# Performance work log

Measured on AMD Instinct MI355X. Metric: run time of the kernel, lower is better.

The kernel has to match this reference:

```python
import jax, jax.numpy as jnp
import numpy as np

HIDDEN = 1024
NUM_HEADS = 16
HEAD = HIDDEN // NUM_HEADS
B, S = 2, 2048


def setup_inputs() -> dict:
    key = jax.random.key(0)
    ks = jax.random.split(key, 7)
    scale = 1.0 / np.sqrt(HIDDEN)
    return {
        "hidden_states": jax.random.normal(ks[0], (B, S, HIDDEN), dtype=jnp.float32),
        "Wq": jax.random.normal(ks[1], (HIDDEN, HIDDEN), dtype=jnp.float32) * scale,
        "bq": jax.random.normal(ks[2], (HIDDEN,), dtype=jnp.float32) * 0.01,
        "Wk": jax.random.normal(ks[3], (HIDDEN, HIDDEN), dtype=jnp.float32) * scale,
        "bk": jax.random.normal(ks[4], (HIDDEN,), dtype=jnp.float32) * 0.01,
        "Wv": jax.random.normal(ks[5], (HIDDEN, HIDDEN), dtype=jnp.float32) * scale,
        "bv": jax.random.normal(ks[6], (HIDDEN,), dtype=jnp.float32) * 0.01,
    }


def _split_heads(x):
    b, s, _ = x.shape
    return x.reshape(b, s, NUM_HEADS, HEAD).transpose(0, 2, 1, 3)  # [B,H,S,D]


def reference(hidden_states, Wq, bq, Wk, bk, Wv, bv):
    # Linear projections (dropout is inference no-op)
    Q = _split_heads(hidden_states @ Wq + bq)
    K = _split_heads(hidden_states @ Wk + bk)
    V = _split_heads(hidden_states @ Wv + bv)
    scores = jnp.einsum("bhqd,bhkd->bhqk", Q, K) / np.sqrt(HEAD).astype(np.float32)
    probs = jax.nn.softmax(scores, axis=-1)
    context = jnp.einsum("bhqk,bhkd->bhqd", probs, V)  # [B,H,S,D]
    return context.transpose(0, 2, 1, 3).reshape(B, S, HIDDEN)
```

## Files before the change

kernel.cpp:

```cpp
#include <hip/hip_runtime.h>
#include <hip/hip_bf16.h>

typedef __bf16 bf16_t;
typedef __bf16 bf16x4v __attribute__((ext_vector_type(4)));
typedef __bf16 bf16x8 __attribute__((ext_vector_type(8)));
typedef float f32x4 __attribute__((ext_vector_type(4)));
typedef float f32x16 __attribute__((ext_vector_type(16)));
typedef unsigned short u16;
typedef unsigned int u32;
typedef u16 u16x8 __attribute__((ext_vector_type(8)));

#define HIDDEN 1024
#define NHEAD 16
#define HEADD 64
#define BATCH 2
#define SEQ 2048
#define TOKENS (BATCH*SEQ)

#define M12F -12.0f
#define M16 {M12F,M12F,M12F,M12F,M12F,M12F,M12F,M12F,M12F,M12F,M12F,M12F,M12F,M12F,M12F,M12F}

__global__ __launch_bounds__(256) void k_transpose_w(const float* __restrict__ Wq,
                                                     const float* __restrict__ Wk,
                                                     const float* __restrict__ Wv,
                                                     bf16_t* __restrict__ wt) {
  int mat = blockIdx.z;
  const float* W = (mat == 0) ? Wq : (mat == 1 ? Wk : Wv);
  bf16_t* dst = wt + (size_t)mat * HIDDEN * HIDDEN;
  __shared__ float tile[32][33];
  int k0 = blockIdx.x * 32, n0 = blockIdx.y * 32;
  int tc = threadIdx.x & 31, tr = threadIdx.x >> 5;
#pragma unroll
  for (int r = 0; r < 32; r += 8)
    tile[tr + r][tc] = W[(size_t)(k0 + tr + r) * HIDDEN + n0 + tc];
  __syncthreads();
#pragma unroll
  for (int r = 0; r < 32; r += 8)
    dst[(size_t)(n0 + tr + r) * HIDDEN + k0 + tc] = (bf16_t)tile[tc][tr + r];
}

__global__ __launch_bounds__(512, 3) void k_gemm_qkv(
    const float* __restrict__ hs, const bf16_t* __restrict__ wt,
    const float* __restrict__ bq, const float* __restrict__ bk,
    const float* __restrict__ bv, bf16_t* __restrict__ Qo,
    bf16_t* __restrict__ Ko, bf16_t* __restrict__ Vo) {
  __shared__ bf16x8 As[2][4 * 128];
  __shared__ bf16x8 Bs[2][4 * 256];
  int t = threadIdx.x;
  int wave = t >> 6, lane = t & 63;
  int m0 = blockIdx.x * 128;
  int nb = blockIdx.y;
  int mat = nb >> 2;
  int n0 = (nb & 3) * 256;
  const bf16_t* Wmat = wt + (size_t)mat * HIDDEN * HIDDEN;
  const float* bias = (mat == 0) ? bq : (mat == 1 ? bk : bv);
  bf16_t* dst = (mat == 0) ? Qo : (mat == 1 ? Ko : Vo);

  int wm = wave >> 2, wn = wave & 3;
  int lrow = lane & 15;
  int lc = lane >> 4;

  f32x4 acc[4][4];
#pragma unroll
  for (int a = 0; a < 4; ++a)
#pragma unroll
    for (int b = 0; b < 4; ++b) acc[a][b] = (f32x4){0.f, 0.f, 0.f, 0.f};

  bf16x8 ra, rb[2];
  auto load_tiles = [&](int kt) {
    int k0 = kt * 32;
    {
      int row = t >> 2, c = t & 3;
      const float* ap = hs + (size_t)(m0 + row) * HIDDEN + k0 + c * 8;
      float4 f0 = *(const float4*)(ap);
      float4 f1 = *(const float4*)(ap + 4);
      bf16x8 v;
      v[0] = (bf16_t)f0.x; v[1] = (bf16_t)f0.y; v[2] = (bf16_t)f0.z; v[3] = (bf16_t)f0.w;
      v[4] = (bf16_t)f1.x; v[5] = (bf16_t)f1.y; v[6] = (bf16_t)f1.z; v[7] = (bf16_t)f1.w;
      ra = v;
    }
#pragma unroll
    for (int u = 0; u < 2; ++u) {
      int id = t + u * 512;
      int row = id >> 2, c = id & 3;
      rb[u] = *(const bf16x8*)(Wmat + (size_t)(n0 + row) * HIDDEN + k0 + c * 8);
    }
  };
  auto store_tiles = [&](int buf) {
    {
      int row = t >> 2, c = t & 3;
      As[buf][c * 128 + (row ^ c)] = ra;
    }
#pragma unroll
    for (int u = 0; u < 2; ++u) {
      int id = t + u * 512;
      int row = id >> 2, c = id & 3;
      Bs[buf][c * 256 + (row ^ c)] = rb[u];
    }
  };

  load_tiles(0);
  store_tiles(0);
  __syncthreads();
  const int NT = HIDDEN / 32;
  int cur = 0;
  for (int kt = 0; kt < NT; ++kt) {
    if (kt + 1 < NT) load_tiles(kt + 1);
    bf16x8 af[4], bfr[4];
#pragma unroll
    for (int fm = 0; fm < 4; ++fm)
      af[fm] = As[cur][lc * 128 + ((wm * 64 + fm * 16 + lrow) ^ lc)];
#pragma unroll
    for (int fn = 0; fn < 4; ++fn)
      bfr[fn] = Bs[cur][lc * 256 + ((wn * 64 + fn * 16 + lrow) ^ lc)];
#pragma unroll
    for (int fm = 0; fm < 4; ++fm)
#pragma unroll
      for (int fn = 0; fn < 4; ++fn)
        acc[fm][fn] = __builtin_amdgcn_mfma_f32_16x16x32_bf16(
            af[fm], bfr[fn], acc[fm][fn], 0, 0, 0);
    if (kt + 1 < NT) store_tiles(cur ^ 1);
    __syncthreads();
    cur ^= 1;
  }

  float scale = (mat == 0) ? 0.18033688011112042f : 1.0f;
#pragma unroll
  for (int fm = 0; fm < 4; ++fm) {
#pragma unroll
    for (int fn = 0; fn < 4; ++fn) {
      int n = n0 + wn * 64 + fn * 16 + (lane & 15);
      float bval = bias[n];
      int h = n >> 6, d = n & 63;
      int mbase = m0 + wm * 64 + fm * 16 + (lane >> 4) * 4;
      int b = mbase >> 11, s = mbase & 2047;
      if (mat == 2) {
        bf16x4v pk;
#pragma unroll
        for (int j = 0; j < 4; ++j) pk[j] = (bf16_t)(acc[fm][fn][j] + bval);
        *(bf16x4v*)(dst + ((size_t)(b * NHEAD + h) * HEADD + d) * SEQ + s) = pk;
      } else {
#pragma unroll
        for (int j = 0; j < 4; ++j) {
          float v = (acc[fm][fn][j] + bval) * scale;
          dst[((size_t)(b * NHEAD + h) * SEQ + (s + j)) * HEADD + d] = (bf16_t)v;
        }
      }
    }
  }
}

__device__ __forceinline__ void gload16(const void* g, void* l) {
  __builtin_amdgcn_global_load_lds((const __attribute__((address_space(1))) u32*)g,
                                   (__attribute__((address_space(3))) u32*)l, 16, 0, 0);
}

#define PACKSUM(sA, sB, PF, L)                                               \
  do {                                                                       \
    u32 u[16];                                                               \
    _Pragma("unroll")                                                        \
    for (int i = 0; i < 8; ++i) {                                            \
      union { bf16_t hh[2]; u32 ww; } c0, c1;                                \
      c0.hh[0] = (bf16_t)sA[2 * i]; c0.hh[1] = (bf16_t)sA[2 * i + 1];        \
      c1.hh[0] = (bf16_t)sB[2 * i]; c1.hh[1] = (bf16_t)sB[2 * i + 1];        \
      u[i] = c0.ww; u[8 + i] = c1.ww;                                        \
    }                                                                        \
    _Pragma("unroll")                                                        \
    for (int i = 0; i < 16; ++i)                                             \
      asm("v_dot2_f32_bf16 %0, %1, %2, %0"                                   \
          : "+v"(L) : "v"(u[i]), "v"(ones_));                                \
    _Pragma("unroll")                                                        \
    for (int gg = 0; gg < 4; ++gg) {                                         \
      u32 a0 = u[4 * gg + 0], b0 = u[4 * gg + 2];                            \
      u32 a1 = u[4 * gg + 1], b1 = u[4 * gg + 3];                            \
      asm("v_permlane32_swap_b32 %0, %1" : "+v"(a0), "+v"(b0));              \
      asm("v_permlane32_swap_b32 %0, %1" : "+v"(a1), "+v"(b1));              \
      union { u32 wv[4]; bf16x8 v; } fu;                                     \
      fu.wv[0] = a0; fu.wv[1] = a1; fu.wv[2] = b0; fu.wv[3] = b1;            \
      PF[gg] = fu.v;                                                         \
    }                                                                        \
  } while (0)

__global__ __launch_bounds__(256, 2) void k_attn(const bf16_t* __restrict__ Q,
                                                 const bf16_t* __restrict__ K,
                                                 const bf16_t* __restrict__ Vt,
                                                 float* __restrict__ out) {
  __shared__ __align__(16) char smem[66560];
  const int t = threadIdx.x;
  const int w = t >> 6, l = t & 63;
  const int g = w >> 1, qh = w & 1;
  const int hi = l >> 5;
  const int l31 = l & 31;
  const int lx = l & 7;

  const int n_hw = blockIdx.x + 16 * blockIdx.y;
  const int work = (n_hw & 7) * 64 + (n_hw >> 3);
  const int qt = work & 15;
  const int bh = work >> 4;
  const int b = bh >> 4, h = bh & 15;
  const char* Kp = (const char*)(K + (size_t)bh * SEQ * HEADD) + (size_t)g * 1024 * 128;
  const char* Vp = (const char*)(Vt + (size_t)bh * HEADD * SEQ) + (size_t)g * 1024 * 2;
  const bf16_t* Qp = Q + (size_t)bh * SEQ * HEADD;

  const int q0w = qt * 128 + qh * 64;

  bf16x8 qa0[4], qa1[4];
#pragma unroll
  for (int ds = 0; ds < 4; ++ds) {
    qa0[ds] = *(const bf16x8*)(Qp + (size_t)(q0w + l31) * HEADD + ds * 16 + hi * 8);
    qa1[ds] = *(const bf16x8*)(Qp + (size_t)(q0w + 32 + l31) * HEADD + ds * 16 + hi * 8);
  }

  f32x16 o00 = (f32x16)(0.f), o01 = (f32x16)(0.f);
  f32x16 o10 = (f32x16)(0.f), o11 = (f32x16)(0.f);
  float l_run0 = 0.f, l_run1 = 0.f;
  const u32 ones_ = 0x3F803F80u;

  char* gK = smem + g * 32768;
  char* gV = gK + 16384;
  const int srow = qh * 32 + (l >> 3);
  const int sg = lx ^ (l >> 3);

  auto stage = [&](int tile, int buf) {
#pragma unroll
    for (int s = 0; s < 4; ++s) {
      int row = srow + 8 * s;
      gload16(Kp + (size_t)(tile * 64 + row) * 128 + sg * 16,
              gK + buf * 8192 + qh * 4096 + s * 1024);
      gload16(Vp + (size_t)row * (SEQ * 2) + tile * 128 + sg * 16,
              gV + buf * 8192 + qh * 4096 + s * 1024);
    }
  };

  stage(0, 0);
  __syncthreads();

  int roff0[4], roff1[4];
#pragma unroll
  for (int ds = 0; ds < 4; ++ds) {
    roff0[ds] = l31 * 128 + ((2 * ds + hi) ^ lx) * 16;
    roff1[ds] = (32 + l31) * 128 + ((2 * ds + hi) ^ lx) * 16;
  }

  const f32x16 minit = M16;
  int cur = 0;
  for (int r = 0; r < 16; ++r) {
    if (r < 15) stage(r + 1, cur ^ 1);
    const char* Kc = gK + cur * 8192;
    const char* Vc = gV + cur * 8192;

    f32x16 s0 = minit, s1 = minit, s2 = minit, s3 = minit;
    __builtin_amdgcn_s_setprio(1);
#pragma unroll
    for (int ds = 0; ds < 4; ++ds) {
      bf16x8 kf0 = *(const bf16x8*)(Kc + roff0[ds]);
      bf16x8 kf1 = *(const bf16x8*)(Kc + roff1[ds]);
      s0 = __builtin_amdgcn_mfma_f32_32x32x16_bf16(kf0, qa0[ds], s0, 0, 0, 0);
      s1 = __builtin_amdgcn_mfma_f32_32x32x16_bf16(kf1, qa0[ds], s1, 0, 0, 0);
      s2 = __builtin_amdgcn_mfma_f32_32x32x16_bf16(kf0, qa1[ds], s2, 0, 0, 0);
      s3 = __builtin_amdgcn_mfma_f32_32x32x16_bf16(kf1, qa1[ds], s3, 0, 0, 0);
    }
    __builtin_amdgcn_s_setprio(0);

#pragma unroll
    for (int i = 0; i < 16; ++i) {
      s0[i] = __builtin_amdgcn_exp2f(s0[i]);
      s1[i] = __builtin_amdgcn_exp2f(s1[i]);
      s2[i] = __builtin_amdgcn_exp2f(s2[i]);
      s3[i] = __builtin_amdgcn_exp2f(s3[i]);
    }

    bf16x8 pf0[4], pf1[4];
    PACKSUM(s0, s1, pf0, l_run0);
    PACKSUM(s2, s3, pf1, l_run1);

    __builtin_amdgcn_s_setprio(1);
#pragma unroll
    for (int kblk = 0; kblk < 4; ++kblk) {
      bf16x8 vf0 = *(const bf16x8*)(Vc + roff0[kblk]);
      bf16x8 vf1 = *(const bf16x8*)(Vc + roff1[kblk]);
      o00 = __builtin_amdgcn_mfma_f32_32x32x16_bf16(vf0, pf0[kblk], o00, 0, 0, 0);
      o01 = __builtin_amdgcn_mfma_f32_32x32x16_bf16(vf1, pf0[kblk], o01, 0, 0, 0);
      o10 = __builtin_amdgcn_mfma_f32_32x32x16_bf16(vf0, pf1[kblk], o10, 0, 0, 0);
      o11 = __builtin_amdgcn_mfma_f32_32x32x16_bf16(vf1, pf1[kblk], o11, 0, 0, 0);
    }
    __builtin_amdgcn_s_setprio(0);
    __syncthreads();
    cur ^= 1;
  }

  float l_h0 = l_run0 + __shfl_xor(l_run0, 32);
  float l_h1 = l_run1 + __shfl_xor(l_run1, 32);
  float* OL = (float*)(smem + g * 32768);
  const int orow0 = qh * 64 + l31;
  const int orow1 = qh * 64 + 32 + l31;
#pragma unroll
  for (int j = 0; j < 16; ++j) {
    int dv0 = (j & 3) + 8 * (j >> 2) + 4 * hi;
    OL[orow0 * 64 + ((dv0 + orow0) & 63)] = o00[j];
    OL[orow0 * 64 + ((dv0 + 32 + orow0) & 63)] = o01[j];
    OL[orow1 * 64 + ((dv0 + orow1) & 63)] = o10[j];
    OL[orow1 * 64 + ((dv0 + 32 + orow1) & 63)] = o11[j];
  }
  float* LL = (float*)(smem + 65536);
  if (hi == 0) {
    LL[g * 128 + orow0] = l_h0;
    LL[g * 128 + orow1] = l_h1;
  }
  __syncthreads();
  {
    int ql = t >> 1;
    int dvb = (t & 1) * 32;
    float inv = 1.0f / (LL[ql] + LL[128 + ql]);
    const float* A = (const float*)smem;
    const float* B = (const float*)(smem + 32768);
    float* op = out + ((size_t)b * SEQ + qt * 128 + ql) * HIDDEN + h * HEADD + dvb;
#pragma unroll
    for (int g4 = 0; g4 < 8; ++g4) {
      f32x4 v4;
#pragma unroll
      for (int e = 0; e < 4; ++e) {
        int dv = dvb + g4 * 4 + e;
        int idx = ql * 64 + ((dv + ql) & 63);
        v4[e] = (A[idx] + B[idx]) * inv;
      }
      *(f32x4*)(op + g4 * 4) = v4;
    }
  }
}

extern "C" void kernel_launch(void* const* d_in, const int* in_sizes, int n_in,
                              void* d_out, int out_size, void* d_ws, size_t ws_size,
                              hipStream_t stream) {
  const float* hs = (const float*)d_in[0];
  const float* Wq = (const float*)d_in[1];
  const float* bq = (const float*)d_in[2];
  const float* Wk = (const float*)d_in[3];
  const float* bk = (const float*)d_in[4];
  const float* Wv = (const float*)d_in[5];
  const float* bv = (const float*)d_in[6];
  float* out = (float*)d_out;
  char* ws = (char*)d_ws;

  const size_t SZ_X = (size_t)TOKENS * HIDDEN * 2;
  const size_t SZ_W = (size_t)3 * HIDDEN * HIDDEN * 2;
  const size_t SZ_P = (size_t)TOKENS * HIDDEN * 2;
  bf16_t* Wt = (bf16_t*)(ws + SZ_X);
  bf16_t* Qb = (bf16_t*)(ws + SZ_X + SZ_W);
  bf16_t* Kb = (bf16_t*)(ws + SZ_X + SZ_W + SZ_P);
  bf16_t* Vb = (bf16_t*)(ws + SZ_X + SZ_W + 2 * SZ_P);

  k_transpose_w<<<dim3(32, 32, 3), 256, 0, stream>>>(Wq, Wk, Wv, Wt);
  k_gemm_qkv<<<dim3(32, 12), 512, 0, stream>>>(hs, Wt, bq, bk, bv, Qb, Kb, Vb);
  k_attn<<<dim3(16, 32), 256, 0, stream>>>(Qb, Kb, Vb, out);
}
```

Before: 97.46 us.

## Halve attention KV tile to 32 keys to fit four blocks per CU

Cuts the per-iteration key tile from 64 to 32 keys, which halves the LDS staging buffers and score registers and lets the launch bound request four blocks per CU instead of two. The V staging layout and swizzle are rewritten for the narrower tile. The final cross-group reduction now runs in two phases through a single LDS buffer, so LDS use fits in about 33KB. In exchange there are twice as many loop iterations and barriers, each with less MFMA work to hide load latency behind.

```diff
diff --git a/kernel.cpp b/kernel.cpp
--- a/kernel.cpp
+++ b/kernel.cpp
@@ -155,22 +155,21 @@
                                    (__attribute__((address_space(3))) u32*)l, 16, 0, 0);
 }
 
-#define PACKSUM(sA, sB, PF, L)                                               \
+#define PACKSUM32(sA, PF, L)                                                 \
   do {                                                                       \
-    u32 u[16];                                                               \
+    u32 u[8];                                                                \
     _Pragma("unroll")                                                        \
     for (int i = 0; i < 8; ++i) {                                            \
-      union { bf16_t hh[2]; u32 ww; } c0, c1;                                \
+      union { bf16_t hh[2]; u32 ww; } c0;                                    \
       c0.hh[0] = (bf16_t)sA[2 * i]; c0.hh[1] = (bf16_t)sA[2 * i + 1];        \
-      c1.hh[0] = (bf16_t)sB[2 * i]; c1.hh[1] = (bf16_t)sB[2 * i + 1];        \
-      u[i] = c0.ww; u[8 + i] = c1.ww;                                        \
+      u[i] = c0.ww;                                                          \
     }                                                                        \
     _Pragma("unroll")                                                        \
-    for (int i = 0; i < 16; ++i)                                             \
+    for (int i = 0; i < 8; ++i)                                              \
       asm("v_dot2_f32_bf16 %0, %1, %2, %0"                                   \
           : "+v"(L) : "v"(u[i]), "v"(ones_));                                \
     _Pragma("unroll")                                                        \
-    for (int gg = 0; gg < 4; ++gg) {                                         \
+    for (int gg = 0; gg < 2; ++gg) {                                         \
       u32 a0 = u[4 * gg + 0], b0 = u[4 * gg + 2];                            \
       u32 a1 = u[4 * gg + 1], b1 = u[4 * gg + 3];                            \
       asm("v_permlane32_swap_b32 %0, %1" : "+v"(a0), "+v"(b0));              \
@@ -181,11 +180,11 @@
     }                                                                        \
   } while (0)
 
-__global__ __launch_bounds__(256, 2) void k_attn(const bf16_t* __restrict__ Q,
+__global__ __launch_bounds__(256, 4) void k_attn(const bf16_t* __restrict__ Q,
                                                  const bf16_t* __restrict__ K,
                                                  const bf16_t* __restrict__ Vt,
                                                  float* __restrict__ out) {
-  __shared__ __align__(16) char smem[66560];
+  __shared__ __align__(16) char smem[33792];
   const int t = threadIdx.x;
   const int w = t >> 6, l = t & 63;
   const int g = w >> 1, qh = w & 1;
@@ -216,69 +215,67 @@
   float l_run0 = 0.f, l_run1 = 0.f;
   const u32 ones_ = 0x3F803F80u;
 
-  char* gK = smem + g * 32768;
-  char* gV = gK + 16384;
-  const int srow = qh * 32 + (l >> 3);
-  const int sg = lx ^ (l >> 3);
+  char* gK = smem + g * 16384;
+  char* gV = gK + 8192;
 
   auto stage = [&](int tile, int buf) {
 #pragma unroll
-    for (int s = 0; s < 4; ++s) {
-      int row = srow + 8 * s;
-      gload16(Kp + (size_t)(tile * 64 + row) * 128 + sg * 16,
-              gK + buf * 8192 + qh * 4096 + s * 1024);
-      gload16(Vp + (size_t)row * (SEQ * 2) + tile * 128 + sg * 16,
-              gV + buf * 8192 + qh * 4096 + s * 1024);
+    for (int s = 0; s < 2; ++s) {
+      int krow = qh * 16 + s * 8 + (l >> 3);
+      gload16(Kp + (size_t)(tile * 32 + krow) * 128 + (lx ^ (krow & 7)) * 16,
+              gK + buf * 4096 + qh * 2048 + s * 1024);
+      int vrow = qh * 32 + s * 16 + (l >> 2);
+      int vg = (l & 3) ^ (vrow & 3);
+      gload16(Vp + (size_t)vrow * (SEQ * 2) + tile * 64 + vg * 16,
+              gV + buf * 4096 + qh * 2048 + s * 1024);
     }
   };
 
   stage(0, 0);
   __syncthreads();
 
-  int roff0[4], roff1[4];
-#pragma unroll
-  for (int ds = 0; ds < 4; ++ds) {
-    roff0[ds] = l31 * 128 + ((2 * ds + hi) ^ lx) * 16;
-    roff1[ds] = (32 + l31) * 128 + ((2 * ds + hi) ^ lx) * 16;
+  int kroff[4], vroff0[2], vroff1[2];
+#pragma unroll
+  for (int ds = 0; ds < 4; ++ds)
+    kroff[ds] = l31 * 128 + ((2 * ds + hi) ^ lx) * 16;
+#pragma unroll
+  for (int kb = 0; kb < 2; ++kb) {
+    vroff0[kb] = l31 * 64 + ((2 * kb + hi) ^ (l31 & 3)) * 16;
+    vroff1[kb] = (32 + l31) * 64 + ((2 * kb + hi) ^ (l31 & 3)) * 16;
   }
 
   const f32x16 minit = M16;
   int cur = 0;
-  for (int r = 0; r < 16; ++r) {
-    if (r < 15) stage(r + 1, cur ^ 1);
-    const char* Kc = gK + cur * 8192;
-    const char* Vc = gV + cur * 8192;
-
-    f32x16 s0 = minit, s1 = minit, s2 = minit, s3 = minit;
+  for (int r = 0; r < 32; ++r) {
+    if (r < 31) stage(r + 1, cur ^ 1);
+    const char* Kc = gK + cur * 4096;
+    const char* Vc = gV + cur * 4096;
+
+    f32x16 s0 = minit, s2 = minit;
     __builtin_amdgcn_s_setprio(1);
 #pragma unroll
     for (int ds = 0; ds < 4; ++ds) {
-      bf16x8 kf0 = *(const bf16x8*)(Kc + roff0[ds]);
-      bf16x8 kf1 = *(const bf16x8*)(Kc + roff1[ds]);
-      s0 = __builtin_amdgcn_mfma_f32_32x32x16_bf16(kf0, qa0[ds], s0, 0, 0, 0);
-      s1 = __builtin_amdgcn_mfma_f32_32x32x16_bf16(kf1, qa0[ds], s1, 0, 0, 0);
-      s2 = __builtin_amdgcn_mfma_f32_32x32x16_bf16(kf0, qa1[ds], s2, 0, 0, 0);
-      s3 = __builtin_amdgcn_mfma_f32_32x32x16_bf16(kf1, qa1[ds], s3, 0, 0, 0);
+      bf16x8 kf = *(const bf16x8*)(Kc + kroff[ds]);
+      s0 = __builtin_amdgcn_mfma_f32_32x32x16_bf16(kf, qa0[ds], s0, 0, 0, 0);
+      s2 = __builtin_amdgcn_mfma_f32_32x32x16_bf16(kf, qa1[ds], s2, 0, 0, 0);
     }
     __builtin_amdgcn_s_setprio(0);
 
 #pragma unroll
     for (int i = 0; i < 16; ++i) {
       s0[i] = __builtin_amdgcn_exp2f(s0[i]);
-      s1[i] = __builtin_amdgcn_exp2f(s1[i]);
       s2[i] = __builtin_amdgcn_exp2f(s2[i]);
-      s3[i] = __builtin_amdgcn_exp2f(s3[i]);
-    }
-
-    bf16x8 pf0[4], pf1[4];
-    PACKSUM(s0, s1, pf0, l_run0);
-    PACKSUM(s2, s3, pf1, l_run1);
+    }
+
+    bf16x8 pf0[2], pf1[2];
+    PACKSUM32(s0, pf0, l_run0);
+    PACKSUM32(s2, pf1, l_run1);
 
     __builtin_amdgcn_s_setprio(1);
 #pragma unroll
-    for (int kblk = 0; kblk < 4; ++kblk) {
-      bf16x8 vf0 = *(const bf16x8*)(Vc + roff0[kblk]);
-      bf16x8 vf1 = *(const bf16x8*)(Vc + roff1[kblk]);
+    for (int kblk = 0; kblk < 2; ++kblk) {
+      bf16x8 vf0 = *(const bf16x8*)(Vc + vroff0[kblk]);
+      bf16x8 vf1 = *(const bf16x8*)(Vc + vroff1[kblk]);
       o00 = __builtin_amdgcn_mfma_f32_32x32x16_bf16(vf0, pf0[kblk], o00, 0, 0, 0);
       o01 = __builtin_amdgcn_mfma_f32_32x32x16_bf16(vf1, pf0[kblk], o01, 0, 0, 0);
       o10 = __builtin_amdgcn_mfma_f32_32x32x16_bf16(vf0, pf1[kblk], o10, 0, 0, 0);
@@ -291,29 +288,38 @@
 
   float l_h0 = l_run0 + __shfl_xor(l_run0, 32);
   float l_h1 = l_run1 + __shfl_xor(l_run1, 32);
-  float* OL = (float*)(smem + g * 32768);
+  float* OL = (float*)smem;
+  float* LL = (float*)(smem + 32768);
   const int orow0 = qh * 64 + l31;
   const int orow1 = qh * 64 + 32 + l31;
-#pragma unroll
-  for (int j = 0; j < 16; ++j) {
-    int dv0 = (j & 3) + 8 * (j >> 2) + 4 * hi;
-    OL[orow0 * 64 + ((dv0 + orow0) & 63)] = o00[j];
-    OL[orow0 * 64 + ((dv0 + 32 + orow0) & 63)] = o01[j];
-    OL[orow1 * 64 + ((dv0 + orow1) & 63)] = o10[j];
-    OL[orow1 * 64 + ((dv0 + 32 + orow1) & 63)] = o11[j];
-  }
-  float* LL = (float*)(smem + 65536);
-  if (hi == 0) {
-    LL[g * 128 + orow0] = l_h0;
-    LL[g * 128 + orow1] = l_h1;
+  if (g == 1) {
+#pragma unroll
+    for (int j = 0; j < 16; ++j) {
+      int dv0 = (j & 3) + 8 * (j >> 2) + 4 * hi;
+      OL[orow0 * 64 + ((dv0 + orow0) & 63)] = o00[j];
+      OL[orow0 * 64 + ((dv0 + 32 + orow0) & 63)] = o01[j];
+      OL[orow1 * 64 + ((dv0 + orow1) & 63)] = o10[j];
+      OL[orow1 * 64 + ((dv0 + 32 + orow1) & 63)] = o11[j];
+    }
+    if (hi == 0) { LL[128 + orow0] = l_h0; LL[128 + orow1] = l_h1; }
+  }
+  __syncthreads();
+  if (g == 0) {
+#pragma unroll
+    for (int j = 0; j < 16; ++j) {
+      int dv0 = (j & 3) + 8 * (j >> 2) + 4 * hi;
+      OL[orow0 * 64 + ((dv0 + orow0) & 63)] += o00[j];
+      OL[orow0 * 64 + ((dv0 + 32 + orow0) & 63)] += o01[j];
+      OL[orow1 * 64 + ((dv0 + orow1) & 63)] += o10[j];
+      OL[orow1 * 64 + ((dv0 + 32 + orow1) & 63)] += o11[j];
+    }
+    if (hi == 0) { LL[orow0] = l_h0; LL[orow1] = l_h1; }
   }
   __syncthreads();
   {
     int ql = t >> 1;
     int dvb = (t & 1) * 32;
     float inv = 1.0f / (LL[ql] + LL[128 + ql]);
-    const float* A = (const float*)smem;
-    const float* B = (const float*)(smem + 32768);
     float* op = out + ((size_t)b * SEQ + qt * 128 + ql) * HIDDEN + h * HEADD + dvb;
 #pragma unroll
     for (int g4 = 0; g4 < 8; ++g4) {
@@ -321,8 +327,7 @@
 #pragma unroll
       for (int e = 0; e < 4; ++e) {
         int dv = dvb + g4 * 4 + e;
-        int idx = ql * 64 + ((dv + ql) & 63);
-        v4[e] = (A[idx] + B[idx]) * inv;
+        v4[e] = OL[ql * 64 + ((dv + ql) & 63)] * inv;
       }
       *(f32x4*)(op + g4 * 4) = v4;
     }
```

New measurement: 229.2 us. 2.35x slower.
